# Kernel tuning notes

Hardware: AMD Instinct MI355X
Metric: run time of the kernel (lower is better)

The kernel has to match this reference:

```python
import jax, jax.numpy as jnp
import numpy as np


def setup_inputs() -> dict:
    key = jax.random.key(0)
    k1, k2, k3, k4 = jax.random.split(key, 4)
    in_f, out_f, rank, tokens = 4096, 4096, 256, 8192
    bound = 1.0 / np.sqrt(in_f)
    x = jax.random.normal(k1, (tokens, in_f), dtype=jnp.float32)
    U = jax.random.uniform(k2, (out_f, rank), dtype=jnp.float32, minval=-bound, maxval=bound)
    V = jax.random.uniform(k3, (rank, in_f), dtype=jnp.float32, minval=-bound, maxval=bound)
    bias = jax.random.uniform(k4, (out_f,), dtype=jnp.float32, minval=-bound, maxval=bound)
    return {"x": x, "U": U, "V": V, "bias": bias}


def reference(x, U, V, bias):
    # Faithful to original: materialize W = U @ V, then F.linear(x, W, bias) = x @ W.T + bias
    W = U @ V                      # [out, in]
    return x @ W.T + bias          # [tokens, out]
```

## Files before the change

kernel.cpp:

```cpp
#include <hip/hip_runtime.h>
#include <stdint.h>

#define TOKENS 8192
#define INF    4096
#define OUTF   4096
#define RANK   256

typedef __attribute__((ext_vector_type(8))) short bf16x8;
typedef __attribute__((ext_vector_type(4))) float f32x4;

__device__ __forceinline__ unsigned short f2bf(float f) {
    union { float f; unsigned int u; } v; v.f = f;
    unsigned int r = v.u + 0x7FFFu + ((v.u >> 16) & 1u);
    return (unsigned short)(r >> 16);
}

__device__ __forceinline__ void gl_lds16(const void* g, void* l) {
    __builtin_amdgcn_global_load_lds(
        (const __attribute__((address_space(1))) unsigned int*)g,
        (__attribute__((address_space(3))) unsigned int*)l, 16, 0, 0);
}

__global__ void cvt4(const float4* __restrict__ in, ushort4* __restrict__ out) {
    int i = blockIdx.x * blockDim.x + threadIdx.x;
    float4 v = in[i];
    ushort4 o;
    o.x = f2bf(v.x); o.y = f2bf(v.y); o.z = f2bf(v.z); o.w = f2bf(v.w);
    out[i] = o;
}

#define G1_BM 32
#define G1_BN 128
#define G1_BK 128
#define A1_STR 136

__global__ __launch_bounds__(512) void gemm1(const float* __restrict__ x,
                                             const unsigned short* __restrict__ Vb,
                                             unsigned short* __restrict__ T) {
    __shared__ __align__(16) unsigned short Axlds[G1_BM * A1_STR];
    __shared__ __align__(16) unsigned short Bvlds[G1_BN * G1_BK];

    const int tid  = threadIdx.x;
    const int lane = tid & 63;
    const int wid  = tid >> 6;
    const int m0   = blockIdx.y * G1_BM;
    const int n0   = blockIdx.x * G1_BN;
    const int l15  = lane & 15;
    const int quad = lane >> 4;

    const int arow = tid >> 4;
    const int aseg = tid & 15;
    const float* xa = x + (size_t)(m0 + arow) * INF + aseg * 8;
    unsigned short* alds_w = &Axlds[arow * A1_STR + aseg * 8];

    const int b_lrow = lane >> 4;
    const int b_pos  = lane & 15;

    f32x4 acc[2];
    acc[0] = (f32x4){0.f, 0.f, 0.f, 0.f};
    acc[1] = (f32x4){0.f, 0.f, 0.f, 0.f};

    for (int kk = 0; kk < INF; kk += G1_BK) {
        #pragma unroll
        for (int j = 0; j < 4; ++j) {
            int r0  = j * 32 + wid * 4;
            int row = r0 + b_lrow;
            int cf  = b_pos ^ (row & 7);
            gl_lds16(Vb + (size_t)(n0 + row) * INF + kk + cf * 8,
                     &Bvlds[r0 * G1_BK]);
        }
        float4 va = *(const float4*)(xa + kk);
        float4 vb = *(const float4*)(xa + kk + 4);
        {
            union { bf16x8 v; unsigned short s[8]; } pk;
            pk.s[0] = f2bf(va.x); pk.s[1] = f2bf(va.y);
            pk.s[2] = f2bf(va.z); pk.s[3] = f2bf(va.w);
            pk.s[4] = f2bf(vb.x); pk.s[5] = f2bf(vb.y);
            pk.s[6] = f2bf(vb.z); pk.s[7] = f2bf(vb.w);
            *(bf16x8*)alds_w = pk.v;
        }
        __syncthreads();
        #pragma unroll
        for (int ks = 0; ks < 4; ++ks) {
            int rr = wid * 16 + l15;
            int p  = (ks * 4 + quad) ^ (rr & 7);
            bf16x8 aV = *(const bf16x8*)&Bvlds[rr * G1_BK + p * 8];
            #pragma unroll
            for (int mt = 0; mt < 2; ++mt) {
                int tr = mt * 16 + l15;
                bf16x8 bx = *(const bf16x8*)&Axlds[tr * A1_STR + ks * 32 + quad * 8];
                acc[mt] = __builtin_amdgcn_mfma_f32_16x16x32_bf16(aV, bx, acc[mt], 0, 0, 0);
            }
        }
        __syncthreads();
    }
    #pragma unroll
    for (int mt = 0; mt < 2; ++mt) {
        int m      = m0 + mt * 16 + l15;
        int n_base = n0 + wid * 16 + quad * 4;
        ushort4 o;
        o.x = f2bf(acc[mt][0]); o.y = f2bf(acc[mt][1]);
        o.z = f2bf(acc[mt][2]); o.w = f2bf(acc[mt][3]);
        *(ushort4*)&T[(size_t)m * RANK + n_base] = o;
    }
}

#define G2_BM 128
#define G2_BN 128
#define G2_BK 64

__global__ __launch_bounds__(256) void gemm2(const unsigned short* __restrict__ Tb,
                                             const unsigned short* __restrict__ Ub,
                                             const float* __restrict__ bias,
                                             float* __restrict__ out) {
    __shared__ __align__(16) unsigned short Tlds[G2_BM * G2_BK];
    __shared__ __align__(16) unsigned short Ulds[G2_BN * G2_BK];

    const int tid  = threadIdx.x;
    const int lane = tid & 63;
    const int wid  = tid >> 6;
    const int wy   = wid >> 1, wx = wid & 1;
    const int m0   = blockIdx.y * G2_BM;
    const int n0   = blockIdx.x * G2_BN;
    const int l15  = lane & 15, quad = lane >> 4;
    const int lrow = lane >> 3;
    const int cf   = (lane & 7) ^ lrow;

    f32x4 acc[4][4];
    #pragma unroll
    for (int i = 0; i < 4; i++)
        #pragma unroll
        for (int j = 0; j < 4; j++) acc[i][j] = (f32x4){0.f, 0.f, 0.f, 0.f};

    for (int kk = 0; kk < RANK; kk += G2_BK) {
        #pragma unroll
        for (int j = 0; j < 4; ++j) {
            int r0 = wid * 32 + j * 8;
            gl_lds16(Tb + (size_t)(m0 + r0 + lrow) * RANK + kk + cf * 8,
                     &Tlds[r0 * G2_BK]);
            gl_lds16(Ub + (size_t)(n0 + r0 + lrow) * RANK + kk + cf * 8,
                     &Ulds[r0 * G2_BK]);
        }
        __syncthreads();
        #pragma unroll
        for (int ks = 0; ks < 2; ++ks) {
            bf16x8 aU[4], bT[4];
            #pragma unroll
            for (int t = 0; t < 4; ++t) {
                int ur = wx * 64 + t * 16 + l15;
                int up = (ks * 4 + quad) ^ (ur & 7);
                aU[t] = *(const bf16x8*)&Ulds[ur * G2_BK + up * 8];
                int tr = wy * 64 + t * 16 + l15;
                int tp = (ks * 4 + quad) ^ (tr & 7);
                bT[t] = *(const bf16x8*)&Tlds[tr * G2_BK + tp * 8];
            }
            #pragma unroll
            for (int nt = 0; nt < 4; ++nt)
                #pragma unroll
                for (int mt = 0; mt < 4; ++mt)
                    acc[nt][mt] = __builtin_amdgcn_mfma_f32_16x16x32_bf16(
                        aU[nt], bT[mt], acc[nt][mt], 0, 0, 0);
        }
        __syncthreads();
    }
    float4 bv[4];
    #pragma unroll
    for (int nt = 0; nt < 4; ++nt)
        bv[nt] = *(const float4*)&bias[n0 + wx * 64 + nt * 16 + quad * 4];
    #pragma unroll
    for (int nt = 0; nt < 4; ++nt) {
        int n_base = n0 + wx * 64 + nt * 16 + quad * 4;
        #pragma unroll
        for (int mt = 0; mt < 4; ++mt) {
            int m = m0 + wy * 64 + mt * 16 + l15;
            float4 v;
            v.x = acc[nt][mt][0] + bv[nt].x;
            v.y = acc[nt][mt][1] + bv[nt].y;
            v.z = acc[nt][mt][2] + bv[nt].z;
            v.w = acc[nt][mt][3] + bv[nt].w;
            *(float4*)&out[(size_t)m * OUTF + n_base] = v;
        }
    }
}

extern "C" void kernel_launch(void* const* d_in, const int* in_sizes, int n_in,
                              void* d_out, int out_size, void* d_ws, size_t ws_size,
                              hipStream_t stream) {
    const float* x    = (const float*)d_in[0];
    const float* U    = (const float*)d_in[1];
    const float* V    = (const float*)d_in[2];
    const float* bias = (const float*)d_in[3];
    float* out = (float*)d_out;

    unsigned short* Vb = (unsigned short*)d_ws;
    unsigned short* Ub = Vb + (size_t)RANK * INF;
    unsigned short* Tb = Ub + (size_t)OUTF * RANK;

    cvt4<<<(RANK * INF / 4) / 256, 256, 0, stream>>>((const float4*)V, (ushort4*)Vb);
    cvt4<<<(OUTF * RANK / 4) / 256, 256, 0, stream>>>((const float4*)U, (ushort4*)Ub);
    gemm1<<<dim3(RANK / G1_BN, TOKENS / G1_BM), 512, 0, stream>>>(x, Vb, Tb);
    gemm2<<<dim3(OUTF / G2_BN, TOKENS / G2_BM), 256, 0, stream>>>(Tb, Ub, bias, out);
}
```

Before: 293.7 us.

## Split-K first GEMM over full rank with fp32 atomics to read x once

Replaces the first GEMM with a split-K variant where each block covers all rank columns over a quarter of the K dimension, accumulating into an fp32 buffer with atomics. A memset and a conversion kernel then produce the bf16 intermediate. This removes the duplicate read of the large fp32 input across rank tiles and raises block count, at the cost of atomic traffic, a memset and an extra conversion pass. It falls back to the old kernel if the workspace is too small.

Result: slower. 362.8 us (+23.5%).

```diff
diff --git a/kernel.cpp b/kernel.cpp
--- a/kernel.cpp
+++ b/kernel.cpp
@@ -29,29 +29,114 @@
     out[i] = o;
 }
 
-#define G1_BM 32
-#define G1_BN 128
-#define G1_BK 128
-#define A1_STR 136
-
-__global__ __launch_bounds__(512) void gemm1(const float* __restrict__ x,
-                                             const unsigned short* __restrict__ Vb,
-                                             unsigned short* __restrict__ T) {
+#define G1_BM  32
+#define G1_BK  64
+#define KSPLIT 4
+#define KSEG   (INF / KSPLIT)
+#define A1_STR 72
+
+__global__ __launch_bounds__(512) void gemm1_sk(const float* __restrict__ x,
+                                                const unsigned short* __restrict__ Vb,
+                                                float* __restrict__ T32) {
+    __shared__ __align__(16) unsigned short Bvlds[RANK * G1_BK];
     __shared__ __align__(16) unsigned short Axlds[G1_BM * A1_STR];
-    __shared__ __align__(16) unsigned short Bvlds[G1_BN * G1_BK];
+
+    const int tid   = threadIdx.x;
+    const int lane  = tid & 63;
+    const int wid   = tid >> 6;
+    const int m0    = blockIdx.y * G1_BM;
+    const int kbase = blockIdx.x * KSEG;
+    const int l15   = lane & 15;
+    const int quad  = lane >> 4;
+
+    const int lrow = lane >> 3;
+    const int cf   = (lane & 7) ^ lrow;
+
+    const int arow = tid >> 4;
+    const int aseg = tid & 15;
+    const float* xa = x + (size_t)(m0 + arow) * INF + kbase + aseg * 4;
+    unsigned short* alds_w = &Axlds[arow * A1_STR + aseg * 4];
+
+    f32x4 acc[2][2];
+    #pragma unroll
+    for (int i = 0; i < 2; i++)
+        #pragma unroll
+        for (int j = 0; j < 2; j++) acc[i][j] = (f32x4){0.f, 0.f, 0.f, 0.f};
+
+    for (int kk = 0; kk < KSEG; kk += G1_BK) {
+        #pragma unroll
+        for (int j = 0; j < 4; ++j) {
+            int r0 = wid * 32 + j * 8;
+            gl_lds16(Vb + (size_t)(r0 + lrow) * INF + kbase + kk + cf * 8,
+                     &Bvlds[r0 * G1_BK]);
+        }
+        float4 v = *(const float4*)(xa + kk);
+        {
+            ushort4 pk;
+            pk.x = f2bf(v.x); pk.y = f2bf(v.y);
+            pk.z = f2bf(v.z); pk.w = f2bf(v.w);
+            *(ushort4*)alds_w = pk;
+        }
+        __syncthreads();
+        #pragma unroll
+        for (int ks = 0; ks < 2; ++ks) {
+            bf16x8 aV[2], bx[2];
+            #pragma unroll
+            for (int nt = 0; nt < 2; ++nt) {
+                int rr = wid * 32 + nt * 16 + l15;
+                int p  = (ks * 4 + quad) ^ (rr & 7);
+                aV[nt] = *(const bf16x8*)&Bvlds[rr * G1_BK + p * 8];
+            }
+            #pragma unroll
+            for (int mt = 0; mt < 2; ++mt) {
+                int tr = mt * 16 + l15;
+                bx[mt] = *(const bf16x8*)&Axlds[tr * A1_STR + ks * 32 + quad * 8];
+            }
+            #pragma unroll
+            for (int mt = 0; mt < 2; ++mt)
+                #pragma unroll
+                for (int nt = 0; nt < 2; ++nt)
+                    acc[mt][nt] = __builtin_amdgcn_mfma_f32_16x16x32_bf16(
+                        aV[nt], bx[mt], acc[mt][nt], 0, 0, 0);
+        }
+        __syncthreads();
+    }
+    #pragma unroll
+    for (int mt = 0; mt < 2; ++mt) {
+        int m = m0 + mt * 16 + l15;
+        #pragma unroll
+        for (int nt = 0; nt < 2; ++nt) {
+            int nb = wid * 32 + nt * 16 + quad * 4;
+            #pragma unroll
+            for (int r = 0; r < 4; ++r)
+                atomicAdd(&T32[(size_t)m * RANK + nb + r], acc[mt][nt][r]);
+        }
+    }
+}
+
+#define F1_BM 32
+#define F1_BN 128
+#define F1_BK 128
+#define F1_STR 136
+
+__global__ __launch_bounds__(512) void gemm1_ns(const float* __restrict__ x,
+                                                const unsigned short* __restrict__ Vb,
+                                                unsigned short* __restrict__ T) {
+    __shared__ __align__(16) unsigned short Axlds[F1_BM * F1_STR];
+    __shared__ __align__(16) unsigned short Bvlds[F1_BN * F1_BK];
 
     const int tid  = threadIdx.x;
     const int lane = tid & 63;
     const int wid  = tid >> 6;
-    const int m0   = blockIdx.y * G1_BM;
-    const int n0   = blockIdx.x * G1_BN;
+    const int m0   = blockIdx.y * F1_BM;
+    const int n0   = blockIdx.x * F1_BN;
     const int l15  = lane & 15;
     const int quad = lane >> 4;
 
     const int arow = tid >> 4;
     const int aseg = tid & 15;
     const float* xa = x + (size_t)(m0 + arow) * INF + aseg * 8;
-    unsigned short* alds_w = &Axlds[arow * A1_STR + aseg * 8];
+    unsigned short* alds_w = &Axlds[arow * F1_STR + aseg * 8];
 
     const int b_lrow = lane >> 4;
     const int b_pos  = lane & 15;
@@ -60,14 +145,14 @@
     acc[0] = (f32x4){0.f, 0.f, 0.f, 0.f};
     acc[1] = (f32x4){0.f, 0.f, 0.f, 0.f};
 
-    for (int kk = 0; kk < INF; kk += G1_BK) {
+    for (int kk = 0; kk < INF; kk += F1_BK) {
         #pragma unroll
         for (int j = 0; j < 4; ++j) {
             int r0  = j * 32 + wid * 4;
             int row = r0 + b_lrow;
-            int cf  = b_pos ^ (row & 7);
-            gl_lds16(Vb + (size_t)(n0 + row) * INF + kk + cf * 8,
-                     &Bvlds[r0 * G1_BK]);
+            int cfx = b_pos ^ (row & 7);
+            gl_lds16(Vb + (size_t)(n0 + row) * INF + kk + cfx * 8,
+                     &Bvlds[r0 * F1_BK]);
         }
         float4 va = *(const float4*)(xa + kk);
         float4 vb = *(const float4*)(xa + kk + 4);
@@ -84,11 +169,11 @@
         for (int ks = 0; ks < 4; ++ks) {
             int rr = wid * 16 + l15;
             int p  = (ks * 4 + quad) ^ (rr & 7);
-            bf16x8 aV = *(const bf16x8*)&Bvlds[rr * G1_BK + p * 8];
+            bf16x8 aV = *(const bf16x8*)&Bvlds[rr * F1_BK + p * 8];
             #pragma unroll
             for (int mt = 0; mt < 2; ++mt) {
                 int tr = mt * 16 + l15;
-                bf16x8 bx = *(const bf16x8*)&Axlds[tr * A1_STR + ks * 32 + quad * 8];
+                bf16x8 bx = *(const bf16x8*)&Axlds[tr * F1_STR + ks * 32 + quad * 8];
                 acc[mt] = __builtin_amdgcn_mfma_f32_16x16x32_bf16(aV, bx, acc[mt], 0, 0, 0);
             }
         }
@@ -192,12 +277,21 @@
     const float* bias = (const float*)d_in[3];
     float* out = (float*)d_out;
 
-    unsigned short* Vb = (unsigned short*)d_ws;
-    unsigned short* Ub = Vb + (size_t)RANK * INF;
-    unsigned short* Tb = Ub + (size_t)OUTF * RANK;
+    unsigned short* Vb  = (unsigned short*)d_ws;
+    unsigned short* Ub  = Vb + (size_t)RANK * INF;
+    unsigned short* Tb  = Ub + (size_t)OUTF * RANK;
+    float*          T32 = (float*)(Tb + (size_t)TOKENS * RANK);
 
     cvt4<<<(RANK * INF / 4) / 256, 256, 0, stream>>>((const float4*)V, (ushort4*)Vb);
     cvt4<<<(OUTF * RANK / 4) / 256, 256, 0, stream>>>((const float4*)U, (ushort4*)Ub);
-    gemm1<<<dim3(RANK / G1_BN, TOKENS / G1_BM), 512, 0, stream>>>(x, Vb, Tb);
+
+    const size_t need = (size_t)16 * 1024 * 1024;
+    if (ws_size >= need) {
+        hipMemsetAsync(T32, 0, (size_t)TOKENS * RANK * sizeof(float), stream);
+        gemm1_sk<<<dim3(KSPLIT, TOKENS / G1_BM), 512, 0, stream>>>(x, Vb, T32);
+        cvt4<<<(TOKENS * RANK / 4) / 256, 256, 0, stream>>>((const float4*)T32, (ushort4*)Tb);
+    } else {
+        gemm1_ns<<<dim3(RANK / F1_BN, TOKENS / F1_BM), 512, 0, stream>>>(x, Vb, Tb);
+    }
     gemm2<<<dim3(OUTF / G2_BN, TOKENS / G2_BM), 256, 0, stream>>>(Tb, Ub, bias, out);
 }
```

## Fuse both low-rank GEMMs into one kernel keeping T in LDS

Applied to the files above, without the earlier changes.

Replaces the two-kernel pipeline with a single fused kernel. Each 32-token block computes its full rank-256 intermediate T, stages it in LDS, then sweeps all 4096 output columns with U fragments loaded straight from global memory into registers. This removes the global round trip for T and one launch, and x loads are software-prefetched. The cost is that V and U are now read per block from global/L2 without LDS staging. There are also only 256 blocks, and the big register footprint may limit occupancy.

After: 362.0 us. 23.3% more time.

```diff
diff --git a/kernel.cpp b/kernel.cpp
--- a/kernel.cpp
+++ b/kernel.cpp
@@ -15,12 +15,6 @@
     return (unsigned short)(r >> 16);
 }
 
-__device__ __forceinline__ void gl_lds16(const void* g, void* l) {
-    __builtin_amdgcn_global_load_lds(
-        (const __attribute__((address_space(1))) unsigned int*)g,
-        (__attribute__((address_space(3))) unsigned int*)l, 16, 0, 0);
-}
-
 __global__ void cvt4(const float4* __restrict__ in, ushort4* __restrict__ out) {
     int i = blockIdx.x * blockDim.x + threadIdx.x;
     float4 v = in[i];
@@ -29,158 +23,133 @@
     out[i] = o;
 }
 
-#define G1_BM 32
-#define G1_BN 128
-#define G1_BK 128
-#define A1_STR 136
+#define BM   32
+#define BK   128
+#define XSTR 136
 
-__global__ __launch_bounds__(512) void gemm1(const float* __restrict__ x,
-                                             const unsigned short* __restrict__ Vb,
-                                             unsigned short* __restrict__ T) {
-    __shared__ __align__(16) unsigned short Axlds[G1_BM * A1_STR];
-    __shared__ __align__(16) unsigned short Bvlds[G1_BN * G1_BK];
+__global__ __launch_bounds__(512, 2) void fused(const float* __restrict__ x,
+                                                const unsigned short* __restrict__ Vb,
+                                                const unsigned short* __restrict__ Ub,
+                                                const float* __restrict__ bias,
+                                                float* __restrict__ out) {
+    __shared__ __align__(16) unsigned short Xlds[BM * XSTR];
+    __shared__ __align__(16) unsigned short T2[2 * 8 * 4 * 16 * 8];
 
     const int tid  = threadIdx.x;
     const int lane = tid & 63;
     const int wid  = tid >> 6;
-    const int m0   = blockIdx.y * G1_BM;
-    const int n0   = blockIdx.x * G1_BN;
     const int l15  = lane & 15;
     const int quad = lane >> 4;
+    const int m0   = blockIdx.x * BM;
 
     const int arow = tid >> 4;
     const int aseg = tid & 15;
     const float* xa = x + (size_t)(m0 + arow) * INF + aseg * 8;
-    unsigned short* alds_w = &Axlds[arow * A1_STR + aseg * 8];
+    unsigned short* xw = &Xlds[arow * XSTR + aseg * 8];
 
-    const int b_lrow = lane >> 4;
-    const int b_pos  = lane & 15;
+    f32x4 acc[2][2];
+    #pragma unroll
+    for (int i = 0; i < 2; i++)
+        #pragma unroll
+        for (int j = 0; j < 2; j++) acc[i][j] = (f32x4){0.f, 0.f, 0.f, 0.f};
 
-    f32x4 acc[2];
-    acc[0] = (f32x4){0.f, 0.f, 0.f, 0.f};
-    acc[1] = (f32x4){0.f, 0.f, 0.f, 0.f};
+    float4 ra = *(const float4*)(xa);
+    float4 rb = *(const float4*)(xa + 4);
 
-    for (int kk = 0; kk < INF; kk += G1_BK) {
-        #pragma unroll
-        for (int j = 0; j < 4; ++j) {
-            int r0  = j * 32 + wid * 4;
-            int row = r0 + b_lrow;
-            int cf  = b_pos ^ (row & 7);
-            gl_lds16(Vb + (size_t)(n0 + row) * INF + kk + cf * 8,
-                     &Bvlds[r0 * G1_BK]);
-        }
-        float4 va = *(const float4*)(xa + kk);
-        float4 vb = *(const float4*)(xa + kk + 4);
+    for (int kk = 0; kk < INF; kk += BK) {
+        __syncthreads();
         {
             union { bf16x8 v; unsigned short s[8]; } pk;
-            pk.s[0] = f2bf(va.x); pk.s[1] = f2bf(va.y);
-            pk.s[2] = f2bf(va.z); pk.s[3] = f2bf(va.w);
-            pk.s[4] = f2bf(vb.x); pk.s[5] = f2bf(vb.y);
-            pk.s[6] = f2bf(vb.z); pk.s[7] = f2bf(vb.w);
-            *(bf16x8*)alds_w = pk.v;
+            pk.s[0] = f2bf(ra.x); pk.s[1] = f2bf(ra.y);
+            pk.s[2] = f2bf(ra.z); pk.s[3] = f2bf(ra.w);
+            pk.s[4] = f2bf(rb.x); pk.s[5] = f2bf(rb.y);
+            pk.s[6] = f2bf(rb.z); pk.s[7] = f2bf(rb.w);
+            *(bf16x8*)xw = pk.v;
+        }
+        if (kk + BK < INF) {
+            ra = *(const float4*)(xa + kk + BK);
+            rb = *(const float4*)(xa + kk + BK + 4);
         }
         __syncthreads();
+
         #pragma unroll
         for (int ks = 0; ks < 4; ++ks) {
-            int rr = wid * 16 + l15;
-            int p  = (ks * 4 + quad) ^ (rr & 7);
-            bf16x8 aV = *(const bf16x8*)&Bvlds[rr * G1_BK + p * 8];
+            bf16x8 aV[2], bx[2];
             #pragma unroll
-            for (int mt = 0; mt < 2; ++mt) {
-                int tr = mt * 16 + l15;
-                bf16x8 bx = *(const bf16x8*)&Axlds[tr * A1_STR + ks * 32 + quad * 8];
-                acc[mt] = __builtin_amdgcn_mfma_f32_16x16x32_bf16(aV, bx, acc[mt], 0, 0, 0);
+            for (int rt = 0; rt < 2; ++rt) {
+                int rr = wid * 32 + rt * 16 + l15;
+                aV[rt] = *(const bf16x8*)&Vb[(size_t)rr * INF + kk + ks * 32 + quad * 8];
             }
+            #pragma unroll
+            for (int tt = 0; tt < 2; ++tt) {
+                int tr = tt * 16 + l15;
+                bx[tt] = *(const bf16x8*)&Xlds[tr * XSTR + ks * 32 + quad * 8];
+            }
+            #pragma unroll
+            for (int rt = 0; rt < 2; ++rt)
+                #pragma unroll
+                for (int tt = 0; tt < 2; ++tt)
+                    acc[rt][tt] = __builtin_amdgcn_mfma_f32_16x16x32_bf16(
+                        aV[rt], bx[tt], acc[rt][tt], 0, 0, 0);
         }
-        __syncthreads();
     }
+
+    __syncthreads();
     #pragma unroll
-    for (int mt = 0; mt < 2; ++mt) {
-        int m      = m0 + mt * 16 + l15;
-        int n_base = n0 + wid * 16 + quad * 4;
-        ushort4 o;
-        o.x = f2bf(acc[mt][0]); o.y = f2bf(acc[mt][1]);
-        o.z = f2bf(acc[mt][2]); o.w = f2bf(acc[mt][3]);
-        *(ushort4*)&T[(size_t)m * RANK + n_base] = o;
-    }
+    for (int rt = 0; rt < 2; ++rt)
+        #pragma unroll
+        for (int tt = 0; tt < 2; ++tt) {
+            int quad2 = rt * 2 + (quad >> 1);
+            int j0    = (quad & 1) * 4;
+            ushort4 o;
+            o.x = f2bf(acc[rt][tt][0]); o.y = f2bf(acc[rt][tt][1]);
+            o.z = f2bf(acc[rt][tt][2]); o.w = f2bf(acc[rt][tt][3]);
+            *(ushort4*)&T2[(((tt * 8 + wid) * 4 + quad2) * 16 + l15) * 8 + j0] = o;
+        }
+    __syncthreads();
+
+    bf16x8 bT[2][8];
+    #pragma unroll
+    for (int tt = 0; tt < 2; ++tt)
+        #pragma unroll
+        for (int ks = 0; ks < 8; ++ks)
+            bT[tt][ks] = *(const bf16x8*)&T2[(((tt * 8 + ks) * 4 + quad) * 16 + l15) * 8];
+
+    const int fb0 = wid * 512;
+    const unsigned short* Urow = Ub + ((size_t)(fb0 + l15)) * RANK + quad * 8;
+
+#define LDU(dst, ft_)                                                      \
+    _Pragma("unroll")                                                      \
+    for (int ks = 0; ks < 8; ++ks)                                         \
+        dst[ks] = *(const bf16x8*)(Urow + (size_t)(ft_) * 16 * RANK + ks * 32);
+
+#define COMPUTE_STORE(au, ft_) {                                           \
+    f32x4 a0 = (f32x4){0.f,0.f,0.f,0.f}, a1 = (f32x4){0.f,0.f,0.f,0.f};    \
+    _Pragma("unroll")                                                      \
+    for (int ks = 0; ks < 8; ++ks) {                                       \
+        a0 = __builtin_amdgcn_mfma_f32_16x16x32_bf16(au[ks], bT[0][ks], a0, 0, 0, 0); \
+        a1 = __builtin_amdgcn_mfma_f32_16x16x32_bf16(au[ks], bT[1][ks], a1, 0, 0, 0); \
+    }                                                                      \
+    int fb = fb0 + (ft_) * 16 + quad * 4;                                  \
+    float4 bv = *(const float4*)&bias[fb];                                 \
+    float4 v0, v1;                                                         \
+    v0.x = a0[0]+bv.x; v0.y = a0[1]+bv.y; v0.z = a0[2]+bv.z; v0.w = a0[3]+bv.w; \
+    v1.x = a1[0]+bv.x; v1.y = a1[1]+bv.y; v1.z = a1[2]+bv.z; v1.w = a1[3]+bv.w; \
+    *(float4*)&out[(size_t)(m0 + l15) * OUTF + fb]      = v0;              \
+    *(float4*)&out[(size_t)(m0 + 16 + l15) * OUTF + fb] = v1;              \
 }
 
-#define G2_BM 128
-#define G2_BN 128
-#define G2_BK 64
-
-__global__ __launch_bounds__(256) void gemm2(const unsigned short* __restrict__ Tb,
-                                             const unsigned short* __restrict__ Ub,
-                                             const float* __restrict__ bias,
-                                             float* __restrict__ out) {
-    __shared__ __align__(16) unsigned short Tlds[G2_BM * G2_BK];
-    __shared__ __align__(16) unsigned short Ulds[G2_BN * G2_BK];
-
-    const int tid  = threadIdx.x;
-    const int lane = tid & 63;
-    const int wid  = tid >> 6;
-    const int wy   = wid >> 1, wx = wid & 1;
-    const int m0   = blockIdx.y * G2_BM;
-    const int n0   = blockIdx.x * G2_BN;
-    const int l15  = lane & 15, quad = lane >> 4;
-    const int lrow = lane >> 3;
-    const int cf   = (lane & 7) ^ lrow;
-
-    f32x4 acc[4][4];
-    #pragma unroll
-    for (int i = 0; i < 4; i++)
-        #pragma unroll
-        for (int j = 0; j < 4; j++) acc[i][j] = (f32x4){0.f, 0.f, 0.f, 0.f};
-
-    for (int kk = 0; kk < RANK; kk += G2_BK) {
-        #pragma unroll
-        for (int j = 0; j < 4; ++j) {
-            int r0 = wid * 32 + j * 8;
-            gl_lds16(Tb + (size_t)(m0 + r0 + lrow) * RANK + kk + cf * 8,
-                     &Tlds[r0 * G2_BK]);
-            gl_lds16(Ub + (size_t)(n0 + r0 + lrow) * RANK + kk + cf * 8,
-                     &Ulds[r0 * G2_BK]);
-        }
-        __syncthreads();
-        #pragma unroll
-        for (int ks = 0; ks < 2; ++ks) {
-            bf16x8 aU[4], bT[4];
-            #pragma unroll
-            for (int t = 0; t < 4; ++t) {
-                int ur = wx * 64 + t * 16 + l15;
-                int up = (ks * 4 + quad) ^ (ur & 7);
-                aU[t] = *(const bf16x8*)&Ulds[ur * G2_BK + up * 8];
-                int tr = wy * 64 + t * 16 + l15;
-                int tp = (ks * 4 + quad) ^ (tr & 7);
-                bT[t] = *(const bf16x8*)&Tlds[tr * G2_BK + tp * 8];
-            }
-            #pragma unroll
-            for (int nt = 0; nt < 4; ++nt)
-                #pragma unroll
-                for (int mt = 0; mt < 4; ++mt)
-                    acc[nt][mt] = __builtin_amdgcn_mfma_f32_16x16x32_bf16(
-                        aU[nt], bT[mt], acc[nt][mt], 0, 0, 0);
-        }
-        __syncthreads();
+    bf16x8 aUa[8], aUb[8];
+    LDU(aUa, 0);
+    #pragma unroll 1
+    for (int ft = 0; ft < 32; ft += 2) {
+        LDU(aUb, ft + 1);
+        COMPUTE_STORE(aUa, ft);
+        if (ft + 2 < 32) { LDU(aUa, ft + 2); }
+        COMPUTE_STORE(aUb, ft + 1);
     }
-    float4 bv[4];
-    #pragma unroll
-    for (int nt = 0; nt < 4; ++nt)
-        bv[nt] = *(const float4*)&bias[n0 + wx * 64 + nt * 16 + quad * 4];
-    #pragma unroll
-    for (int nt = 0; nt < 4; ++nt) {
-        int n_base = n0 + wx * 64 + nt * 16 + quad * 4;
-        #pragma unroll
-        for (int mt = 0; mt < 4; ++mt) {
-            int m = m0 + wy * 64 + mt * 16 + l15;
-            float4 v;
-            v.x = acc[nt][mt][0] + bv[nt].x;
-            v.y = acc[nt][mt][1] + bv[nt].y;
-            v.z = acc[nt][mt][2] + bv[nt].z;
-            v.w = acc[nt][mt][3] + bv[nt].w;
-            *(float4*)&out[(size_t)m * OUTF + n_base] = v;
-        }
-    }
+#undef LDU
+#undef COMPUTE_STORE
 }
 
 extern "C" void kernel_launch(void* const* d_in, const int* in_sizes, int n_in,
@@ -194,10 +163,8 @@
 
     unsigned short* Vb = (unsigned short*)d_ws;
     unsigned short* Ub = Vb + (size_t)RANK * INF;
-    unsigned short* Tb = Ub + (size_t)OUTF * RANK;
 
     cvt4<<<(RANK * INF / 4) / 256, 256, 0, stream>>>((const float4*)V, (ushort4*)Vb);
     cvt4<<<(OUTF * RANK / 4) / 256, 256, 0, stream>>>((const float4*)U, (ushort4*)Ub);
-    gemm1<<<dim3(RANK / G1_BN, TOKENS / G1_BM), 512, 0, stream>>>(x, Vb, Tb);
-    gemm2<<<dim3(OUTF / G2_BN, TOKENS / G2_BM), 256, 0, stream>>>(Tb, Ub, bias, out);
+    fused<<<TOKENS / BM, 512, 0, stream>>>(x, Vb, Ub, bias, out);
 }
```
